# Optimization experiments

Hardware: AMD Instinct MI355X
Metric: run time of the kernel (lower is better)

Reference implementation:

```python
import jax, jax.numpy as jnp
import numpy as np

DIM = 1024
HEADS = 16
DIM_HEAD = 64
INNER = HEADS * DIM_HEAD
EPS = 1e-6


def elu_feature_map(t):
    # F.elu(x) + 1
    return jnp.where(t > 0, t + 1.0, jnp.exp(t))


def setup_inputs() -> dict:
    key = jax.random.key(0)
    k1, k2, k3, k4 = jax.random.split(key, 4)
    B, N = 4, 8192
    x = jax.random.normal(k1, (B, N, DIM), dtype=jnp.float32)
    s_in = 1.0 / np.sqrt(DIM)
    s_out = 1.0 / np.sqrt(INNER)
    Wqkv = jax.random.uniform(k2, (DIM, 3 * INNER), dtype=jnp.float32, minval=-s_in, maxval=s_in)
    Wout = jax.random.uniform(k3, (INNER, DIM), dtype=jnp.float32, minval=-s_out, maxval=s_out)
    bout = jax.random.uniform(k4, (DIM,), dtype=jnp.float32, minval=-s_out, maxval=s_out)
    return {"x": x, "Wqkv": Wqkv, "Wout": Wout, "bout": bout}


def reference(x, Wqkv, Wout, bout):
    B, N, D = x.shape
    qkv = x @ Wqkv  # [B,N,3*INNER]
    q, k, v = jnp.split(qkv, 3, axis=-1)
    # b n (h d) -> b h n d
    resh = lambda t: t.reshape(B, N, HEADS, DIM_HEAD).transpose(0, 2, 1, 3)
    q, k, v = resh(q), resh(k), resh(v)
    q = elu_feature_map(q)
    k = elu_feature_map(k)
    kv = jnp.einsum('bhnd,bhnf->bhdf', k, v)          # [B,H,d,d]
    k_sum = k.sum(axis=-2)                             # [B,H,d]
    qkv_out = jnp.einsum('bhnd,bhdf->bhnf', q, kv)    # [B,H,N,d]
    q_k_sum = jnp.einsum('bhnd,bhd->bhn', q, k_sum)   # [B,H,N]
    out = qkv_out / (q_k_sum[..., None] + EPS)
    out = out.transpose(0, 2, 1, 3).reshape(B, N, INNER)  # b h n d -> b n (h d)
    return out @ Wout + bout
```

## Files before the change

### kernel.cpp

```cpp
#include <hip/hip_runtime.h>
#include <hip/hip_bf16.h>
#include <math.h>


typedef unsigned short ushort_t;
typedef __attribute__((ext_vector_type(8))) short s8v;
typedef __attribute__((ext_vector_type(4))) float f32x4;

#define MFMA(a,b,c) __builtin_amdgcn_mfma_f32_16x16x32_bf16((a),(b),(c),0,0,0)

typedef __attribute__((address_space(3))) unsigned int as3_u32;
typedef __attribute__((address_space(1))) const unsigned int as1_u32c;

__device__ __forceinline__ void g2l16(const void* g, void* l) {
    __builtin_amdgcn_global_load_lds((as1_u32c*)g, (as3_u32*)l, 16, 0, 0);
}

__device__ __forceinline__ float bf2f(ushort_t u) {
    union { float f; unsigned v; } x; x.v = ((unsigned)u) << 16; return x.f;
}
__device__ __forceinline__ ushort_t f2bf(float f) {
    union { float f; unsigned v; } x; x.f = f;
    unsigned r = x.v + 0x7fffu + ((x.v >> 16) & 1u);
    return (ushort_t)(r >> 16);
}
__device__ __forceinline__ float elu1(float t) { return t > 0.0f ? t + 1.0f : expf(t); }

__global__ __launch_bounds__(256) void k_prep(
    const float* __restrict__ x, const float* __restrict__ Wqkv,
    const float* __restrict__ Wout, ushort_t* __restrict__ xb,
    ushort_t* __restrict__ WqkvT, ushort_t* __restrict__ WoutT,
    float* __restrict__ zeroreg)
{
    const int bid = blockIdx.x, t = threadIdx.x;
    if (bid < 4096) {
        const float* W; ushort_t* WT; int K, N, idx;
        if (bid < 3072) { W = Wqkv; WT = WqkvT; K = 1024; N = 3072; idx = bid; }
        else            { W = Wout; WT = WoutT; K = 1024; N = 1024; idx = bid - 3072; }
        const int k0 = (idx & 31) * 32, n0 = (idx >> 5) * 32;
        __shared__ float s[32][33];
        const int kr = t >> 3, n4 = (t & 7) * 4;
        float4 v = *(const float4*)(W + (size_t)(k0 + kr) * N + n0 + n4);
        s[kr][n4 + 0] = v.x; s[kr][n4 + 1] = v.y; s[kr][n4 + 2] = v.z; s[kr][n4 + 3] = v.w;
        __syncthreads();
        const int nr = kr, k4 = n4;
        unsigned lo = (unsigned)f2bf(s[k4 + 0][nr]) | ((unsigned)f2bf(s[k4 + 1][nr]) << 16);
        unsigned hi = (unsigned)f2bf(s[k4 + 2][nr]) | ((unsigned)f2bf(s[k4 + 3][nr]) << 16);
        *(uint2*)(WT + (size_t)(n0 + nr) * K + k0 + k4) = make_uint2(lo, hi);
    } else if (bid < 20480) {
        const size_t i = (size_t)(bid - 4096) * 256 + t;
        const float4* p = (const float4*)x;
        float4 a = p[i * 2], b = p[i * 2 + 1];
        uint4 o;
        o.x = (unsigned)f2bf(a.x) | ((unsigned)f2bf(a.y) << 16);
        o.y = (unsigned)f2bf(a.z) | ((unsigned)f2bf(a.w) << 16);
        o.z = (unsigned)f2bf(b.x) | ((unsigned)f2bf(b.y) << 16);
        o.w = (unsigned)f2bf(b.z) | ((unsigned)f2bf(b.w) << 16);
        *(uint4*)(xb + i * 8) = o;
    } else {
        float4* dst = (float4*)zeroreg;
        const float4 z4 = {0.f, 0.f, 0.f, 0.f};
        for (int i = (bid - 20480) * 256 + t; i < 263168; i += 8192)
            dst[i] = z4;
    }
}

template<int MODE>
__global__ __launch_bounds__(512, 2) void k_gemm(
    const ushort_t* __restrict__ A, const ushort_t* __restrict__ B,
    ushort_t* __restrict__ obf, const float* __restrict__ bout, float* __restrict__ of)
{
    constexpr int ASZ  = 256 * 64;
    constexpr int BUFS = 2 * ASZ;
    constexpr int NBN  = (MODE == 0) ? 12 : 4;
    constexpr int CH   = (128 * NBN) / 8;
    __shared__ ushort_t lds[2 * BUFS];

    const int t = threadIdx.x, l = t & 63, w = t >> 6;
    const int wr = w >> 2, wc = w & 3;
    const int orig = blockIdx.x;
    const int wg   = (orig & 7) * CH + (orig >> 3);
    const size_t m0 = (size_t)(wg / NBN) * 256;
    const size_t n0 = (size_t)(wg % NBN) * 256;

    f32x4 acc[8][4];
    const f32x4 z = {0.f, 0.f, 0.f, 0.f};
#pragma unroll
    for (int i = 0; i < 8; i++)
#pragma unroll
        for (int j = 0; j < 4; j++) acc[i][j] = z;

    const int lr  = l >> 3;
    const int lco = ((l & 7) ^ lr) << 3;
    const ushort_t* gA = A + (m0 + (size_t)(32 * w) + lr) * 1024 + lco;
    const ushort_t* gB = B + (n0 + (size_t)(32 * w) + lr) * 1024 + lco;
    const int la15 = l & 15;
    const int exo  = (((l >> 4) ^ (l & 7)) << 3);

#pragma unroll
    for (int i = 0; i < 4; i++)
        g2l16(gA + (size_t)(8 * i) * 1024, &lds[(w * 4 + i) * 512]);
#pragma unroll
    for (int i = 0; i < 4; i++)
        g2l16(gB + (size_t)(8 * i) * 1024, &lds[ASZ + (w * 4 + i) * 512]);
    asm volatile("s_waitcnt vmcnt(0)" ::: "memory");
    __builtin_amdgcn_sched_barrier(0);
    __builtin_amdgcn_s_barrier();
    __builtin_amdgcn_sched_barrier(0);

    for (int T = 0; T < 16; ++T) {
        const int base  = (T & 1) * BUFS;
        const int nbase = BUFS - base;

        if (T < 15) {
            const size_t k1 = (size_t)(T + 1) * 64;
#pragma unroll
            for (int i = 0; i < 4; i++)
                g2l16(gA + (size_t)(8 * i) * 1024 + k1, &lds[nbase + (w * 4 + i) * 512]);
#pragma unroll
            for (int i = 0; i < 4; i++)
                g2l16(gB + (size_t)(8 * i) * 1024 + k1, &lds[nbase + ASZ + (w * 4 + i) * 512]);
        }

        s8v af[8], bf[4];
#pragma unroll
        for (int nf = 0; nf < 4; nf++)
            bf[nf] = *(const s8v*)&lds[base + ASZ + (wc * 64 + nf * 16 + la15) * 64 + exo];
#pragma unroll
        for (int mf = 0; mf < 8; mf++)
            af[mf] = *(const s8v*)&lds[base + (wr * 128 + mf * 16 + la15) * 64 + exo];
        __builtin_amdgcn_s_setprio(1);
#pragma unroll
        for (int mf = 0; mf < 8; mf++)
#pragma unroll
            for (int nf = 0; nf < 4; nf++)
                acc[mf][nf] = MFMA(af[mf], bf[nf], acc[mf][nf]);
        __builtin_amdgcn_s_setprio(0);
#pragma unroll
        for (int nf = 0; nf < 4; nf++)
            bf[nf] = *(const s8v*)&lds[base + ASZ + (wc * 64 + nf * 16 + la15) * 64 + (32 ^ exo)];
#pragma unroll
        for (int mf = 0; mf < 8; mf++)
            af[mf] = *(const s8v*)&lds[base + (wr * 128 + mf * 16 + la15) * 64 + (32 ^ exo)];
        __builtin_amdgcn_s_setprio(1);
#pragma unroll
        for (int mf = 0; mf < 8; mf++)
#pragma unroll
            for (int nf = 0; nf < 4; nf++)
                acc[mf][nf] = MFMA(af[mf], bf[nf], acc[mf][nf]);
        __builtin_amdgcn_s_setprio(0);

        if (T < 15) {
            __builtin_amdgcn_sched_barrier(0);
            asm volatile("s_waitcnt vmcnt(0)" ::: "memory");
            __builtin_amdgcn_sched_barrier(0);
            __builtin_amdgcn_s_barrier();
            __builtin_amdgcn_sched_barrier(0);
        }
    }

    const int r4 = (l >> 4) * 4;
    if (MODE == 0) {
#pragma unroll
        for (int mf = 0; mf < 8; mf++)
#pragma unroll
            for (int nf = 0; nf < 4; nf++) {
                const size_t colb = n0 + wc * 64 + nf * 16;
                const bool feat = colb < 2048;
#pragma unroll
                for (int r = 0; r < 4; r++) {
                    const size_t row = m0 + wr * 128 + mf * 16 + r4 + r;
                    float v = acc[mf][nf][r];
                    obf[row * 3072 + colb + la15] = f2bf(feat ? elu1(v) : v);
                }
            }
    } else {
#pragma unroll
        for (int mf = 0; mf < 8; mf++)
#pragma unroll
            for (int nf = 0; nf < 4; nf++) {
                const size_t col = n0 + wc * 64 + nf * 16 + la15;
                const float bo = bout[col];
#pragma unroll
                for (int r = 0; r < 4; r++) {
                    const size_t row = m0 + wr * 128 + mf * 16 + r4 + r;
                    of[row * 1024 + col] = acc[mf][nf][r] + bo;
                }
            }
    }
}

#define KST 136
__global__ __launch_bounds__(256) void k_kv(
    const ushort_t* __restrict__ qkv, float* __restrict__ kv, float* __restrict__ ksum)
{
    __shared__ ushort_t kT[64 * KST];
    __shared__ ushort_t vT[64 * KST];
    __shared__ float ksl[64];
    const int t = threadIdx.x, l = t & 63, w = t >> 6;
    const int wr = w >> 1, wc = w & 1;
    const int h = blockIdx.x;
    const int b = blockIdx.z;
    const ushort_t* qkvb = qkv + (size_t)b * 8192 * 3072;
    float* kvh = kv + ((size_t)b * 16 + h) * 4096;
    float* ksh = ksum + (size_t)b * 1024 + h * 64;
    const int n00 = blockIdx.y * 1024;
    const f32x4 z = {0.f, 0.f, 0.f, 0.f};
    f32x4 acc[2][2] = {{z, z}, {z, z}};
    float ksloc[4] = {0.f, 0.f, 0.f, 0.f};
    const int sd0 = (t & 15) * 4;
    const int tg  = t >> 4;
    if (t < 64) ksl[t] = 0.f;

    for (int c = 0; c < 8; c++) {
        __syncthreads();
        const int n0 = n00 + c * 128;
#pragma unroll
        for (int jj = 0; jj < 2; jj++) {
            const int nb = tg * 8 + jj * 4;
            ushort4 kw[4], vw[4];
#pragma unroll
            for (int j = 0; j < 4; j++) {
                const ushort_t* kp = qkvb + (size_t)(n0 + nb + j) * 3072 + 1024 + h * 64 + sd0;
                kw[j] = *(const ushort4*)kp;
                vw[j] = *(const ushort4*)(kp + 1024);
            }
#pragma unroll
            for (int j = 0; j < 4; j++) {
                ksloc[0] += bf2f(kw[j].x); ksloc[1] += bf2f(kw[j].y);
                ksloc[2] += bf2f(kw[j].z); ksloc[3] += bf2f(kw[j].w);
            }
            *(ushort4*)&kT[(sd0 + 0) * KST + nb] = make_ushort4(kw[0].x, kw[1].x, kw[2].x, kw[3].x);
            *(ushort4*)&kT[(sd0 + 1) * KST + nb] = make_ushort4(kw[0].y, kw[1].y, kw[2].y, kw[3].y);
            *(ushort4*)&kT[(sd0 + 2) * KST + nb] = make_ushort4(kw[0].z, kw[1].z, kw[2].z, kw[3].z);
            *(ushort4*)&kT[(sd0 + 3) * KST + nb] = make_ushort4(kw[0].w, kw[1].w, kw[2].w, kw[3].w);
            *(ushort4*)&vT[(sd0 + 0) * KST + nb] = make_ushort4(vw[0].x, vw[1].x, vw[2].x, vw[3].x);
            *(ushort4*)&vT[(sd0 + 1) * KST + nb] = make_ushort4(vw[0].y, vw[1].y, vw[2].y, vw[3].y);
            *(ushort4*)&vT[(sd0 + 2) * KST + nb] = make_ushort4(vw[0].z, vw[1].z, vw[2].z, vw[3].z);
            *(ushort4*)&vT[(sd0 + 3) * KST + nb] = make_ushort4(vw[0].w, vw[1].w, vw[2].w, vw[3].w);
        }
        __syncthreads();
#pragma unroll
        for (int kb = 0; kb < 128; kb += 32) {
            s8v af[2], bfr[2];
#pragma unroll
            for (int ma = 0; ma < 2; ma++) {
                int d = wr * 32 + ma * 16 + (l & 15);
                af[ma] = *(const s8v*)&kT[d * KST + kb + (l >> 4) * 8];
            }
#pragma unroll
            for (int fb = 0; fb < 2; fb++) {
                int f = wc * 32 + fb * 16 + (l & 15);
                bfr[fb] = *(const s8v*)&vT[f * KST + kb + (l >> 4) * 8];
            }
#pragma unroll
            for (int ma = 0; ma < 2; ma++)
#pragma unroll
                for (int fb = 0; fb < 2; fb++)
                    acc[ma][fb] = MFMA(af[ma], bfr[fb], acc[ma][fb]);
        }
    }
    atomicAdd(&ksl[sd0 + 0], ksloc[0]); atomicAdd(&ksl[sd0 + 1], ksloc[1]);
    atomicAdd(&ksl[sd0 + 2], ksloc[2]); atomicAdd(&ksl[sd0 + 3], ksloc[3]);
    __syncthreads();
    if (t < 64) atomicAdd(&ksh[t], ksl[t]);
#pragma unroll
    for (int ma = 0; ma < 2; ma++)
#pragma unroll
        for (int fb = 0; fb < 2; fb++)
#pragma unroll
            for (int r = 0; r < 4; r++) {
                int d = wr * 32 + ma * 16 + (l >> 4) * 4 + r;
                int f = wc * 32 + fb * 16 + (l & 15);
                atomicAdd(&kvh[f * 64 + d], acc[ma][fb][r]);
            }
}

#define AST 72
#define OST 520
__global__ __launch_bounds__(256) void k_apply(
    const ushort_t* __restrict__ qkv, const float* __restrict__ kv,
    const float* __restrict__ ksum, ushort_t* __restrict__ attn)
{
    __shared__ ushort_t kvb[64 * AST];
    __shared__ ushort_t obuf[32 * OST];
    const int t = threadIdx.x, l = t & 63, w = t >> 6;
    const int la15 = l & 15;
    const int row0 = blockIdx.x * 32;
    const int b = row0 >> 13;
    const f32x4 z = {0.f, 0.f, 0.f, 0.f};

    for (int hh = 0; hh < 8; hh++) {
        const int h = blockIdx.y * 8 + hh;
        const float* kvh = kv + ((size_t)b * 16 + h) * 4096;
        const float* ksh = ksum + (size_t)b * 1024 + h * 64;
        __syncthreads();
        {
            const int f = t >> 2, d0 = (t & 3) * 16;
            const float* src = kvh + f * 64 + d0;
            s8v v0, v1;
#pragma unroll
            for (int j = 0; j < 8; j++) {
                v0[j] = (short)f2bf(src[j]);
                v1[j] = (short)f2bf(src[j + 8]);
            }
            *(s8v*)&kvb[f * AST + d0]     = v0;
            *(s8v*)&kvb[f * AST + d0 + 8] = v1;
        }
        __syncthreads();
        float ksv[16];
        {
            const float* kp = ksh + (l >> 4) * 8;
            *(float4*)&ksv[0]  = *(const float4*)(kp);
            *(float4*)&ksv[4]  = *(const float4*)(kp + 4);
            *(float4*)&ksv[8]  = *(const float4*)(kp + 32);
            *(float4*)&ksv[12] = *(const float4*)(kp + 36);
        }
        f32x4 acc[2] = {z, z};
        float pd[2] = {0.f, 0.f};
#pragma unroll
        for (int ks = 0; ks < 2; ks++) {
            const int f = w * 16 + la15;
            s8v bfr = *(const s8v*)&kvb[f * AST + ks * 32 + (l >> 4) * 8];
#pragma unroll
            for (int ma = 0; ma < 2; ma++) {
                int row = row0 + ma * 16 + la15;
                s8v afr = *(const s8v*)(qkv + (size_t)row * 3072 + h * 64 + ks * 32 + (l >> 4) * 8);
#pragma unroll
                for (int j = 0; j < 8; j++)
                    pd[ma] += bf2f((ushort_t)afr[j]) * ksv[ks * 8 + j];
                acc[ma] = MFMA(afr, bfr, acc[ma]);
            }
        }
#pragma unroll
        for (int ma = 0; ma < 2; ma++) {
            pd[ma] += __shfl_xor(pd[ma], 16, 64);
            pd[ma] += __shfl_xor(pd[ma], 32, 64);
        }
#pragma unroll
        for (int ma = 0; ma < 2; ma++)
#pragma unroll
            for (int r = 0; r < 4; r++) {
                int lrow = (l >> 4) * 4 + r;
                float dot = __shfl(pd[ma], lrow, 64);
                float dv = 1.f / (dot + 1e-6f);
                int orow = ma * 16 + lrow;
                int ocol = hh * 64 + w * 16 + la15;
                obuf[orow * OST + ocol] = f2bf(acc[ma][r] * dv);
            }
    }
    __syncthreads();
    {
        const int row = t >> 3;
        const int c0  = (t & 7) * 8;
        ushort_t* dst = attn + (size_t)(row0 + row) * 1024 + blockIdx.y * 512;
#pragma unroll
        for (int i = 0; i < 8; i++) {
            const int col = c0 + i * 64;
            *(uint4*)(dst + col) = *(const uint4*)&obuf[row * OST + col];
        }
    }
}

extern "C" void kernel_launch(void* const* d_in, const int* in_sizes, int n_in,
                              void* d_out, int out_size, void* d_ws, size_t ws_size,
                              hipStream_t stream) {
    const float* x    = (const float*)d_in[0];
    const float* Wqkv = (const float*)d_in[1];
    const float* Wout = (const float*)d_in[2];
    const float* bout = (const float*)d_in[3];
    float* out = (float*)d_out;
    char* ws = (char*)d_ws;

    ushort_t* WqkvT = (ushort_t*)(ws + 0);
    ushort_t* WoutT = (ushort_t*)(ws + 6291456);
    float*    kv    = (float*)(ws + 8388608);
    float*    ksum  = (float*)(ws + 12582912);
    ushort_t* xb    = (ushort_t*)(ws + 12599296);
    ushort_t* qkv   = (ushort_t*)(ws + 79708160);
    ushort_t* attn  = (ushort_t*)(ws + 281034752);

    k_prep<<<20512, 256, 0, stream>>>(x, Wqkv, Wout, xb, WqkvT, WoutT, kv);

    k_gemm<0><<<1536, 512, 0, stream>>>(xb, WqkvT, qkv, nullptr, nullptr);
    k_kv<<<dim3(16, 8, 4), 256, 0, stream>>>(qkv, kv, ksum);
    k_apply<<<dim3(1024, 2), 256, 0, stream>>>(qkv, kv, ksum, attn);
    k_gemm<1><<<512, 512, 0, stream>>>(attn, WoutT, nullptr, bout, out);
}
```

Measured before the change: 479.2 us.

## Use three-stage K-pipeline with 32-wide K tiles in GEMM kernel

Switches the GEMM main loop from a double-buffered 64-wide K tile to a triple-buffered 32-wide K tile, prefetching two stages ahead and waiting with vmcnt(4) so one stage of loads stays in flight across each barrier. The LDS swizzle is redone for 32-element rows, and A fragments are loaded one at a time and interleaved with the MFMAs to lower register pressure. The loop now takes twice as many barriers with less MFMA work between them.

```diff
diff --git a/kernel.cpp b/kernel.cpp
--- a/kernel.cpp
+++ b/kernel.cpp
@@ -70,11 +70,11 @@
     const ushort_t* __restrict__ A, const ushort_t* __restrict__ B,
     ushort_t* __restrict__ obf, const float* __restrict__ bout, float* __restrict__ of)
 {
-    constexpr int ASZ  = 256 * 64;
+    constexpr int ASZ  = 256 * 32;
     constexpr int BUFS = 2 * ASZ;
     constexpr int NBN  = (MODE == 0) ? 12 : 4;
     constexpr int CH   = (128 * NBN) / 8;
-    __shared__ ushort_t lds[2 * BUFS];
+    __shared__ ushort_t lds[3 * BUFS];
 
     const int t = threadIdx.x, l = t & 63, w = t >> 6;
     const int wr = w >> 2, wc = w & 3;
@@ -90,73 +90,61 @@
 #pragma unroll
         for (int j = 0; j < 4; j++) acc[i][j] = z;
 
-    const int lr  = l >> 3;
-    const int lco = ((l & 7) ^ lr) << 3;
-    const ushort_t* gA = A + (m0 + (size_t)(32 * w) + lr) * 1024 + lco;
-    const ushort_t* gB = B + (n0 + (size_t)(32 * w) + lr) * 1024 + lco;
+    const int swz = (((l & 3) ^ ((l >> 3) & 3)) << 3);
+    const ushort_t* gA = A + (m0 + (size_t)(32 * w) + (l >> 2)) * 1024 + swz;
+    const ushort_t* gB = B + (n0 + (size_t)(32 * w) + (l >> 2)) * 1024 + swz;
+    const int dA = (32 * w) * 32;
+
     const int la15 = l & 15;
-    const int exo  = (((l >> 4) ^ (l & 7)) << 3);
-
-#pragma unroll
-    for (int i = 0; i < 4; i++)
-        g2l16(gA + (size_t)(8 * i) * 1024, &lds[(w * 4 + i) * 512]);
-#pragma unroll
-    for (int i = 0; i < 4; i++)
-        g2l16(gB + (size_t)(8 * i) * 1024, &lds[ASZ + (w * 4 + i) * 512]);
-    asm volatile("s_waitcnt vmcnt(0)" ::: "memory");
+    const int exo  = (((l >> 4) ^ ((la15 >> 1) & 3)) << 3);
+
+    g2l16(gA,                  &lds[dA]);
+    g2l16(gA + 16 * 1024,      &lds[dA + 16 * 32]);
+    g2l16(gB,                  &lds[ASZ + dA]);
+    g2l16(gB + 16 * 1024,      &lds[ASZ + dA + 16 * 32]);
+    g2l16(gA + 32,             &lds[BUFS + dA]);
+    g2l16(gA + 16 * 1024 + 32, &lds[BUFS + dA + 16 * 32]);
+    g2l16(gB + 32,             &lds[BUFS + ASZ + dA]);
+    g2l16(gB + 16 * 1024 + 32, &lds[BUFS + ASZ + dA + 16 * 32]);
+    asm volatile("s_waitcnt vmcnt(4)" ::: "memory");
     __builtin_amdgcn_sched_barrier(0);
     __builtin_amdgcn_s_barrier();
     __builtin_amdgcn_sched_barrier(0);
 
-    for (int T = 0; T < 16; ++T) {
-        const int base  = (T & 1) * BUFS;
-        const int nbase = BUFS - base;
-
-        if (T < 15) {
-            const size_t k1 = (size_t)(T + 1) * 64;
-#pragma unroll
-            for (int i = 0; i < 4; i++)
-                g2l16(gA + (size_t)(8 * i) * 1024 + k1, &lds[nbase + (w * 4 + i) * 512]);
-#pragma unroll
-            for (int i = 0; i < 4; i++)
-                g2l16(gB + (size_t)(8 * i) * 1024 + k1, &lds[nbase + ASZ + (w * 4 + i) * 512]);
-        }
-
-        s8v af[8], bf[4];
+    int cur = 0, nx2 = 2 * BUFS;
+    for (int T = 0; T < 32; ++T) {
+        if (T < 30) {
+            const size_t k2 = (size_t)(T + 2) * 32;
+            g2l16(gA + k2,             &lds[nx2 + dA]);
+            g2l16(gA + 16 * 1024 + k2, &lds[nx2 + dA + 16 * 32]);
+            g2l16(gB + k2,             &lds[nx2 + ASZ + dA]);
+            g2l16(gB + 16 * 1024 + k2, &lds[nx2 + ASZ + dA + 16 * 32]);
+        }
+
+        s8v bf[4];
 #pragma unroll
         for (int nf = 0; nf < 4; nf++)
-            bf[nf] = *(const s8v*)&lds[base + ASZ + (wc * 64 + nf * 16 + la15) * 64 + exo];
-#pragma unroll
-        for (int mf = 0; mf < 8; mf++)
-            af[mf] = *(const s8v*)&lds[base + (wr * 128 + mf * 16 + la15) * 64 + exo];
-        __builtin_amdgcn_s_setprio(1);
-#pragma unroll
-        for (int mf = 0; mf < 8; mf++)
+            bf[nf] = *(const s8v*)&lds[cur + ASZ + (wc * 64 + nf * 16 + la15) * 32 + exo];
+#pragma unroll
+        for (int mf = 0; mf < 8; mf++) {
+            s8v af = *(const s8v*)&lds[cur + (wr * 128 + mf * 16 + la15) * 32 + exo];
+            __builtin_amdgcn_s_setprio(1);
 #pragma unroll
             for (int nf = 0; nf < 4; nf++)
-                acc[mf][nf] = MFMA(af[mf], bf[nf], acc[mf][nf]);
-        __builtin_amdgcn_s_setprio(0);
-#pragma unroll
-        for (int nf = 0; nf < 4; nf++)
-            bf[nf] = *(const s8v*)&lds[base + ASZ + (wc * 64 + nf * 16 + la15) * 64 + (32 ^ exo)];
-#pragma unroll
-        for (int mf = 0; mf < 8; mf++)
-            af[mf] = *(const s8v*)&lds[base + (wr * 128 + mf * 16 + la15) * 64 + (32 ^ exo)];
-        __builtin_amdgcn_s_setprio(1);
-#pragma unroll
-        for (int mf = 0; mf < 8; mf++)
-#pragma unroll
-            for (int nf = 0; nf < 4; nf++)
-                acc[mf][nf] = MFMA(af[mf], bf[nf], acc[mf][nf]);
-        __builtin_amdgcn_s_setprio(0);
-
-        if (T < 15) {
+                acc[mf][nf] = MFMA(af, bf[nf], acc[mf][nf]);
+            __builtin_amdgcn_s_setprio(0);
+        }
+
+        if (T < 31) {
             __builtin_amdgcn_sched_barrier(0);
-            asm volatile("s_waitcnt vmcnt(0)" ::: "memory");
+            if (T < 30) asm volatile("s_waitcnt vmcnt(4)" ::: "memory");
+            else        asm volatile("s_waitcnt vmcnt(0)" ::: "memory");
             __builtin_amdgcn_sched_barrier(0);
             __builtin_amdgcn_s_barrier();
             __builtin_amdgcn_sched_barrier(0);
         }
+        cur = (cur == 2 * BUFS) ? 0 : cur + BUFS;
+        nx2 = (nx2 == 2 * BUFS) ? 0 : nx2 + BUFS;
     }
 
     const int r4 = (l >> 4) * 4;
```

Result: slower. 491.3 us (+2.5%).

## Shrink GEMM tiles to 128x128 with single-buffered LDS and more blocks

Applied to the files above, without the earlier changes.

Both GEMMs drop from a 256x256 tile with 8 waves and double-buffered LDS prefetch to a 128x128 tile with 4 waves and a single LDS buffer. Each K step is loaded synchronously and then computed. The grid grows fourfold and launch bounds allow 4 blocks per CU, so more blocks can hide latency in place of software pipelining. In exchange, the smaller tiles reuse data less and loads no longer overlap with MFMA work inside a block.

```diff
diff --git a/kernel.cpp b/kernel.cpp
--- a/kernel.cpp
+++ b/kernel.cpp
@@ -66,27 +66,27 @@
 }
 
 template<int MODE>
-__global__ __launch_bounds__(512, 2) void k_gemm(
+__global__ __launch_bounds__(256, 4) void k_gemm(
     const ushort_t* __restrict__ A, const ushort_t* __restrict__ B,
     ushort_t* __restrict__ obf, const float* __restrict__ bout, float* __restrict__ of)
 {
-    constexpr int ASZ  = 256 * 64;
-    constexpr int BUFS = 2 * ASZ;
-    constexpr int NBN  = (MODE == 0) ? 12 : 4;
-    constexpr int CH   = (128 * NBN) / 8;
-    __shared__ ushort_t lds[2 * BUFS];
+    constexpr int ASZ = 128 * 64;
+    constexpr int NBN = (MODE == 0) ? 24 : 8;
+    constexpr int CH  = (256 * NBN) / 8;
+    __shared__ ushort_t As[ASZ];
+    __shared__ ushort_t Bs[ASZ];
 
     const int t = threadIdx.x, l = t & 63, w = t >> 6;
-    const int wr = w >> 2, wc = w & 3;
+    const int wr = w >> 1, wc = w & 1;
     const int orig = blockIdx.x;
     const int wg   = (orig & 7) * CH + (orig >> 3);
-    const size_t m0 = (size_t)(wg / NBN) * 256;
-    const size_t n0 = (size_t)(wg % NBN) * 256;
-
-    f32x4 acc[8][4];
+    const size_t m0 = (size_t)(wg / NBN) * 128;
+    const size_t n0 = (size_t)(wg % NBN) * 128;
+
+    f32x4 acc[4][4];
     const f32x4 z = {0.f, 0.f, 0.f, 0.f};
 #pragma unroll
-    for (int i = 0; i < 8; i++)
+    for (int i = 0; i < 4; i++)
 #pragma unroll
         for (int j = 0; j < 4; j++) acc[i][j] = z;
 
@@ -97,93 +97,66 @@
     const int la15 = l & 15;
     const int exo  = (((l >> 4) ^ (l & 7)) << 3);
 
-#pragma unroll
-    for (int i = 0; i < 4; i++)
-        g2l16(gA + (size_t)(8 * i) * 1024, &lds[(w * 4 + i) * 512]);
-#pragma unroll
-    for (int i = 0; i < 4; i++)
-        g2l16(gB + (size_t)(8 * i) * 1024, &lds[ASZ + (w * 4 + i) * 512]);
-    asm volatile("s_waitcnt vmcnt(0)" ::: "memory");
-    __builtin_amdgcn_sched_barrier(0);
-    __builtin_amdgcn_s_barrier();
-    __builtin_amdgcn_sched_barrier(0);
-
     for (int T = 0; T < 16; ++T) {
-        const int base  = (T & 1) * BUFS;
-        const int nbase = BUFS - base;
-
-        if (T < 15) {
-            const size_t k1 = (size_t)(T + 1) * 64;
-#pragma unroll
-            for (int i = 0; i < 4; i++)
-                g2l16(gA + (size_t)(8 * i) * 1024 + k1, &lds[nbase + (w * 4 + i) * 512]);
-#pragma unroll
-            for (int i = 0; i < 4; i++)
-                g2l16(gB + (size_t)(8 * i) * 1024 + k1, &lds[nbase + ASZ + (w * 4 + i) * 512]);
-        }
-
-        s8v af[8], bf[4];
-#pragma unroll
-        for (int nf = 0; nf < 4; nf++)
-            bf[nf] = *(const s8v*)&lds[base + ASZ + (wc * 64 + nf * 16 + la15) * 64 + exo];
-#pragma unroll
-        for (int mf = 0; mf < 8; mf++)
-            af[mf] = *(const s8v*)&lds[base + (wr * 128 + mf * 16 + la15) * 64 + exo];
-        __builtin_amdgcn_s_setprio(1);
-#pragma unroll
-        for (int mf = 0; mf < 8; mf++)
+        const size_t k0 = (size_t)T * 64;
+#pragma unroll
+        for (int i = 0; i < 4; i++) {
+            g2l16(gA + (size_t)(8 * i) * 1024 + k0, &As[(w * 4 + i) * 512]);
+            g2l16(gB + (size_t)(8 * i) * 1024 + k0, &Bs[(w * 4 + i) * 512]);
+        }
+        asm volatile("s_waitcnt vmcnt(0)" ::: "memory");
+        __builtin_amdgcn_sched_barrier(0);
+        __builtin_amdgcn_s_barrier();
+        __builtin_amdgcn_sched_barrier(0);
+
+#pragma unroll
+        for (int kh = 0; kh < 2; kh++) {
+            const int eo = (kh << 5) ^ exo;
+            s8v af[4], bf[4];
 #pragma unroll
             for (int nf = 0; nf < 4; nf++)
-                acc[mf][nf] = MFMA(af[mf], bf[nf], acc[mf][nf]);
-        __builtin_amdgcn_s_setprio(0);
-#pragma unroll
-        for (int nf = 0; nf < 4; nf++)
-            bf[nf] = *(const s8v*)&lds[base + ASZ + (wc * 64 + nf * 16 + la15) * 64 + (32 ^ exo)];
-#pragma unroll
-        for (int mf = 0; mf < 8; mf++)
-            af[mf] = *(const s8v*)&lds[base + (wr * 128 + mf * 16 + la15) * 64 + (32 ^ exo)];
-        __builtin_amdgcn_s_setprio(1);
-#pragma unroll
-        for (int mf = 0; mf < 8; mf++)
-#pragma unroll
-            for (int nf = 0; nf < 4; nf++)
-                acc[mf][nf] = MFMA(af[mf], bf[nf], acc[mf][nf]);
-        __builtin_amdgcn_s_setprio(0);
-
-        if (T < 15) {
-            __builtin_amdgcn_sched_barrier(0);
-            asm volatile("s_waitcnt vmcnt(0)" ::: "memory");
-            __builtin_amdgcn_sched_barrier(0);
-            __builtin_amdgcn_s_barrier();
-            __builtin_amdgcn_sched_barrier(0);
-        }
+                bf[nf] = *(const s8v*)&Bs[(wc * 64 + nf * 16 + la15) * 64 + eo];
+#pragma unroll
+            for (int mf = 0; mf < 4; mf++)
+                af[mf] = *(const s8v*)&As[(wr * 64 + mf * 16 + la15) * 64 + eo];
+            __builtin_amdgcn_s_setprio(1);
+#pragma unroll
+            for (int mf = 0; mf < 4; mf++)
+#pragma unroll
+                for (int nf = 0; nf < 4; nf++)
+                    acc[mf][nf] = MFMA(af[mf], bf[nf], acc[mf][nf]);
+            __builtin_amdgcn_s_setprio(0);
+        }
+        __builtin_amdgcn_sched_barrier(0);
+        __builtin_amdgcn_s_barrier();
+        __builtin_amdgcn_sched_barrier(0);
     }
 
     const int r4 = (l >> 4) * 4;
     if (MODE == 0) {
 #pragma unroll
-        for (int mf = 0; mf < 8; mf++)
+        for (int mf = 0; mf < 4; mf++)
 #pragma unroll
             for (int nf = 0; nf < 4; nf++) {
                 const size_t colb = n0 + wc * 64 + nf * 16;
                 const bool feat = colb < 2048;
 #pragma unroll
                 for (int r = 0; r < 4; r++) {
-                    const size_t row = m0 + wr * 128 + mf * 16 + r4 + r;
+                    const size_t row = m0 + wr * 64 + mf * 16 + r4 + r;
                     float v = acc[mf][nf][r];
                     obf[row * 3072 + colb + la15] = f2bf(feat ? elu1(v) : v);
                 }
             }
     } else {
 #pragma unroll
-        for (int mf = 0; mf < 8; mf++)
+        for (int mf = 0; mf < 4; mf++)
 #pragma unroll
             for (int nf = 0; nf < 4; nf++) {
                 const size_t col = n0 + wc * 64 + nf * 16 + la15;
                 const float bo = bout[col];
 #pragma unroll
                 for (int r = 0; r < 4; r++) {
-                    const size_t row = m0 + wr * 128 + mf * 16 + r4 + r;
+                    const size_t row = m0 + wr * 64 + mf * 16 + r4 + r;
                     of[row * 1024 + col] = acc[mf][nf][r] + bo;
                 }
             }
@@ -382,8 +355,8 @@
 
     k_prep<<<20512, 256, 0, stream>>>(x, Wqkv, Wout, xb, WqkvT, WoutT, kv);
 
-    k_gemm<0><<<1536, 512, 0, stream>>>(xb, WqkvT, qkv, nullptr, nullptr);
+    k_gemm<0><<<6144, 256, 0, stream>>>(xb, WqkvT, qkv, nullptr, nullptr);
     k_kv<<<dim3(16, 8, 4), 256, 0, stream>>>(qkv, kv, ksum);
     k_apply<<<dim3(1024, 2), 256, 0, stream>>>(qkv, kv, ksum, attn);
-    k_gemm<1><<<512, 512, 0, stream>>>(attn, WoutT, nullptr, bout, out);
-}
+    k_gemm<1><<<2048, 256, 0, stream>>>(attn, WoutT, nullptr, bout, out);
+}
```

After: 481.0 us. About the same (+0.4%).

## Replace QKV GEMM with smaller 128x128 single-buffered tile kernel

Applied to the files above, without the earlier changes.

The QKV projection GEMM moves from the shared 256x256 double-buffered, 512-thread template to a dedicated 128x128 tile kernel with 256 threads, a single LDS buffer and four blocks per CU. The output GEMM keeps the original design as a separate non-template kernel. The goal is more blocks in flight, with higher occupancy hiding latency. The cost is lower per-tile data reuse, roughly doubled global/LDS traffic, and no overlap of loads with MFMA, since each k-step waits on its loads before computing.

```diff
diff --git a/kernel.cpp b/kernel.cpp
--- a/kernel.cpp
+++ b/kernel.cpp
@@ -65,14 +65,95 @@
     }
 }
 
-template<int MODE>
-__global__ __launch_bounds__(512, 2) void k_gemm(
+__global__ __launch_bounds__(256, 4) void k_gemm1(
     const ushort_t* __restrict__ A, const ushort_t* __restrict__ B,
-    ushort_t* __restrict__ obf, const float* __restrict__ bout, float* __restrict__ of)
+    ushort_t* __restrict__ obf)
+{
+    constexpr int ASZ = 128 * 64;
+    constexpr int NBN = 24;
+    constexpr int CH  = (256 * NBN) / 8;
+    __shared__ ushort_t As[ASZ];
+    __shared__ ushort_t Bs[ASZ];
+
+    const int t = threadIdx.x, l = t & 63, w = t >> 6;
+    const int wr = w >> 1, wc = w & 1;
+    const int orig = blockIdx.x;
+    const int wg   = (orig & 7) * CH + (orig >> 3);
+    const size_t m0 = (size_t)(wg / NBN) * 128;
+    const size_t n0 = (size_t)(wg % NBN) * 128;
+
+    f32x4 acc[4][4];
+    const f32x4 z = {0.f, 0.f, 0.f, 0.f};
+#pragma unroll
+    for (int i = 0; i < 4; i++)
+#pragma unroll
+        for (int j = 0; j < 4; j++) acc[i][j] = z;
+
+    const int lr  = l >> 3;
+    const int lco = ((l & 7) ^ lr) << 3;
+    const ushort_t* gA = A + (m0 + (size_t)(32 * w) + lr) * 1024 + lco;
+    const ushort_t* gB = B + (n0 + (size_t)(32 * w) + lr) * 1024 + lco;
+    const int la15 = l & 15;
+    const int exo  = (((l >> 4) ^ (l & 7)) << 3);
+
+    for (int T = 0; T < 16; ++T) {
+        const size_t k0 = (size_t)T * 64;
+#pragma unroll
+        for (int i = 0; i < 4; i++) {
+            g2l16(gA + (size_t)(8 * i) * 1024 + k0, &As[(w * 4 + i) * 512]);
+            g2l16(gB + (size_t)(8 * i) * 1024 + k0, &Bs[(w * 4 + i) * 512]);
+        }
+        asm volatile("s_waitcnt vmcnt(0)" ::: "memory");
+        __builtin_amdgcn_sched_barrier(0);
+        __builtin_amdgcn_s_barrier();
+        __builtin_amdgcn_sched_barrier(0);
+
+#pragma unroll
+        for (int kh = 0; kh < 2; kh++) {
+            const int eo = (kh << 5) ^ exo;
+            s8v af[4], bf[4];
+#pragma unroll
+            for (int nf = 0; nf < 4; nf++)
+                bf[nf] = *(const s8v*)&Bs[(wc * 64 + nf * 16 + la15) * 64 + eo];
+#pragma unroll
+            for (int mf = 0; mf < 4; mf++)
+                af[mf] = *(const s8v*)&As[(wr * 64 + mf * 16 + la15) * 64 + eo];
+            __builtin_amdgcn_s_setprio(1);
+#pragma unroll
+            for (int mf = 0; mf < 4; mf++)
+#pragma unroll
+                for (int nf = 0; nf < 4; nf++)
+                    acc[mf][nf] = MFMA(af[mf], bf[nf], acc[mf][nf]);
+            __builtin_amdgcn_s_setprio(0);
+        }
+        __builtin_amdgcn_sched_barrier(0);
+        __builtin_amdgcn_s_barrier();
+        __builtin_amdgcn_sched_barrier(0);
+    }
+
+    const int r4 = (l >> 4) * 4;
+#pragma unroll
+    for (int mf = 0; mf < 4; mf++)
+#pragma unroll
+        for (int nf = 0; nf < 4; nf++) {
+            const size_t colb = n0 + wc * 64 + nf * 16;
+            const bool feat = colb < 2048;
+#pragma unroll
+            for (int r = 0; r < 4; r++) {
+                const size_t row = m0 + wr * 64 + mf * 16 + r4 + r;
+                float v = acc[mf][nf][r];
+                obf[row * 3072 + colb + la15] = f2bf(feat ? elu1(v) : v);
+            }
+        }
+}
+
+__global__ __launch_bounds__(512, 2) void k_gemm2(
+    const ushort_t* __restrict__ A, const ushort_t* __restrict__ B,
+    const float* __restrict__ bout, float* __restrict__ of)
 {
     constexpr int ASZ  = 256 * 64;
     constexpr int BUFS = 2 * ASZ;
-    constexpr int NBN  = (MODE == 0) ? 12 : 4;
+    constexpr int NBN  = 4;
     constexpr int CH   = (128 * NBN) / 8;
     __shared__ ushort_t lds[2 * BUFS];
 
@@ -160,34 +241,18 @@
     }
 
     const int r4 = (l >> 4) * 4;
-    if (MODE == 0) {
-#pragma unroll
-        for (int mf = 0; mf < 8; mf++)
-#pragma unroll
-            for (int nf = 0; nf < 4; nf++) {
-                const size_t colb = n0 + wc * 64 + nf * 16;
-                const bool feat = colb < 2048;
-#pragma unroll
-                for (int r = 0; r < 4; r++) {
-                    const size_t row = m0 + wr * 128 + mf * 16 + r4 + r;
-                    float v = acc[mf][nf][r];
-                    obf[row * 3072 + colb + la15] = f2bf(feat ? elu1(v) : v);
-                }
-            }
-    } else {
-#pragma unroll
-        for (int mf = 0; mf < 8; mf++)
-#pragma unroll
-            for (int nf = 0; nf < 4; nf++) {
-                const size_t col = n0 + wc * 64 + nf * 16 + la15;
-                const float bo = bout[col];
-#pragma unroll
-                for (int r = 0; r < 4; r++) {
-                    const size_t row = m0 + wr * 128 + mf * 16 + r4 + r;
-                    of[row * 1024 + col] = acc[mf][nf][r] + bo;
-                }
-            }
-    }
+#pragma unroll
+    for (int mf = 0; mf < 8; mf++)
+#pragma unroll
+        for (int nf = 0; nf < 4; nf++) {
+            const size_t col = n0 + wc * 64 + nf * 16 + la15;
+            const float bo = bout[col];
+#pragma unroll
+            for (int r = 0; r < 4; r++) {
+                const size_t row = m0 + wr * 128 + mf * 16 + r4 + r;
+                of[row * 1024 + col] = acc[mf][nf][r] + bo;
+            }
+        }
 }
 
 #define KST 136
@@ -382,8 +447,8 @@
 
     k_prep<<<20512, 256, 0, stream>>>(x, Wqkv, Wout, xb, WqkvT, WoutT, kv);
 
-    k_gemm<0><<<1536, 512, 0, stream>>>(xb, WqkvT, qkv, nullptr, nullptr);
+    k_gemm1<<<6144, 256, 0, stream>>>(xb, WqkvT, qkv);
     k_kv<<<dim3(16, 8, 4), 256, 0, stream>>>(qkv, kv, ksum);
     k_apply<<<dim3(1024, 2), 256, 0, stream>>>(qkv, kv, ksum, attn);
-    k_gemm<1><<<512, 512, 0, stream>>>(attn, WoutT, nullptr, bout, out);
-}
+    k_gemm2<<<512, 512, 0, stream>>>(attn, WoutT, bout, out);
+}
```

Result: no change. 479.1 us (-0.0%).
